# Kernel optimization log

Measured on AMD Instinct MI355X. Metric: run time of the kernel, lower is better.

The kernel has to match this reference:

```python
import jax, jax.numpy as jnp
import numpy as np

HEADS = 8
CPH = 32


def _rel_pos_indices(h, w):
    # same construction as the torch buffer, done statically in numpy
    coords = np.stack(np.meshgrid(np.arange(h), np.arange(w), indexing='ij')).reshape(2, -1)  # [2, N]
    rel = coords[:, :, None] - coords[:, None, :]  # [2, N, N]
    idx = (rel[0] + h - 1) * (2 * w - 1) + (rel[1] + w - 1)  # [N, N]
    return jnp.asarray(idx, dtype=jnp.int32)


def setup_inputs() -> dict:
    key = jax.random.key(0)
    ks = jax.random.split(key, 6)
    B, C, H, W = 2, 256, 48, 48
    emb = HEADS * CPH  # 256
    x = jax.random.normal(ks[0], (B, C, H, W), dtype=jnp.float32)
    # GDN params (kept positive so sqrt is well-defined)
    gdn_beta = jnp.ones((C,), dtype=jnp.float32)
    gdn_gamma = 0.1 * jnp.eye(C, dtype=jnp.float32) + 0.001 * jax.random.uniform(ks[1], (C, C), dtype=jnp.float32)
    w_qkv = 0.02 * jax.random.normal(ks[2], (3 * emb, C), dtype=jnp.float32)
    w_out = 0.02 * jax.random.normal(ks[3], (C, emb), dtype=jnp.float32)
    b_out = jnp.zeros((C,), dtype=jnp.float32)
    table_size = (2 * H - 1) * (2 * W - 1)
    rel_bias_table = 0.02 * jax.random.normal(ks[4], (table_size, HEADS), dtype=jnp.float32)
    return {"x": x, "gdn_beta": gdn_beta, "gdn_gamma": gdn_gamma,
            "w_qkv": w_qkv, "w_out": w_out, "b_out": b_out,
            "rel_bias_table": rel_bias_table}


def reference(x, gdn_beta, gdn_gamma, w_qkv, w_out, b_out, rel_bias_table):
    B, C, H, W = x.shape
    N = H * W
    emb = HEADS * CPH
    scale = CPH ** (-0.5)

    # GDN: y = x / sqrt(beta + gamma * x^2)  (1x1 conv over channels of x^2)
    norm = jnp.einsum('bchw,dc->bdhw', x * x, gdn_gamma) + gdn_beta[None, :, None, None]
    xn = x / jnp.sqrt(norm)

    # flatten spatial, channels last: [B, N, C]
    t = xn.reshape(B, C, N).transpose(0, 2, 1)

    # qkv projection (no bias)
    qkv = (t @ w_qkv.T).reshape(B, N, 3, HEADS, CPH).transpose(2, 0, 3, 1, 4)  # [3, B, h, N, d]
    q, k, v = qkv[0], qkv[1], qkv[2]

    attn = jnp.einsum('bhnd,bhmd->bhnm', q, k) * scale  # [B, h, N, N]

    # gathered relative position bias: [h, N, N]
    idx = _rel_pos_indices(H, W)  # [N, N], static ints
    bias = rel_bias_table[idx.reshape(-1)].reshape(N, N, HEADS).transpose(2, 0, 1)
    attn = jax.nn.softmax(attn + bias[None], axis=-1)

    # NOTE: faithful to the original quirk — reshape (B, h, N, d) directly
    # to (B, N, C) with NO head/seq transpose, exactly like the torch code.
    res = jnp.einsum('bhnm,bhmd->bhnd', attn, v).reshape(B, N, emb)

    out = res @ w_out.T + b_out  # [B, N, C]
    return out.transpose(0, 2, 1).reshape(B, C, H, W)
```

## Files before the change

### kernel.cpp

```cpp
#include <hip/hip_runtime.h>
#include <cstdint>
#include <cstddef>

typedef __attribute__((ext_vector_type(8))) short short8;
typedef __attribute__((ext_vector_type(4))) float floatx4;
typedef __attribute__((ext_vector_type(4))) unsigned short ushort4v;

#define NB 2
#define NPIX 2304
#define TBL 9025
#define TBLP 9032
#define L2E 1.4426950408889634f
#define QSCALE 0.17677669529663689f

__device__ __forceinline__ float b2f(unsigned short u) {
  union { unsigned int i; float f; } v; v.i = ((unsigned int)u) << 16; return v.f;
}
__device__ __forceinline__ unsigned short f2b(float f) {
  union { float f; unsigned int i; } v; v.f = f;
  return (unsigned short)((v.i + 0x7fffu + ((v.i >> 16) & 1u)) >> 16);
}
__device__ __forceinline__ unsigned int f2b2_fast(float lo, float hi) {
  union { float f; unsigned int i; } a, b; a.f = lo; b.f = hi;
  return ((a.i + 0x8000u) >> 16) | (((b.i + 0x8000u) >> 16) << 16);
}

__global__ __launch_bounds__(256) void prep_k(
    const float* __restrict__ gamma, const float* __restrict__ wqkv,
    const float* __restrict__ wout, const float* __restrict__ table,
    unsigned short* __restrict__ gb, unsigned short* __restrict__ qb,
    unsigned short* __restrict__ wb, float* __restrict__ tbf)
{
  int i = blockIdx.x * 256 + threadIdx.x;
  if (i < 65536)  gb[i] = f2b(gamma[i]);
  if (i < 196608) qb[i] = f2b(wqkv[i]);
  if (i < 65536)  wb[i] = f2b(wout[i]);
  if (i < TBL * 8) {
    int e = i >> 3, h = i & 7;
    tbf[(size_t)h * TBLP + e] = table[i] * L2E;
  }
}

template<int MODE>
__global__ __launch_bounds__(256) void gemm_k(
    const unsigned short* __restrict__ A,
    const void* __restrict__ Bv,
    const float* __restrict__ vec,
    unsigned short* __restrict__ o0,
    unsigned short* __restrict__ o1,
    unsigned short* __restrict__ o2,
    float* __restrict__ of)
{
  __shared__ unsigned short Al[64][40];
  __shared__ unsigned short Bl[64][40];
  const float* __restrict__ X = (const float*)Bv;
  const unsigned short* __restrict__ Bw = (const unsigned short*)Bv;

  const int n0 = blockIdx.x * 64;
  const int m0 = blockIdx.y * 64;
  const int b  = blockIdx.z;
  const int tid = threadIdx.x;
  const int wave = tid >> 6, lane = tid & 63;
  const int wm = wave >> 1, wn = wave & 1;
  const int lm = lane & 15, quad = lane >> 4;

  floatx4 acc[2][2] = {};

  for (int k0 = 0; k0 < 256; k0 += 32) {
    __syncthreads();
    {
      int ml = tid >> 2, ko = (tid & 3) * 8;
      *(short8*)&Al[ml][ko] = *(const short8*)&A[(size_t)(m0 + ml) * 256 + k0 + ko];
    }
    if (MODE == 0) {
      int kk = tid >> 3, n8 = (tid & 7) * 8;
      const float* xr = &X[((size_t)(b * 256 + k0 + kk)) * NPIX + n0 + n8];
      float4 x0 = *(const float4*)xr;
      float4 x1 = *(const float4*)(xr + 4);
      Bl[n8 + 0][kk] = f2b(x0.x * x0.x);
      Bl[n8 + 1][kk] = f2b(x0.y * x0.y);
      Bl[n8 + 2][kk] = f2b(x0.z * x0.z);
      Bl[n8 + 3][kk] = f2b(x0.w * x0.w);
      Bl[n8 + 4][kk] = f2b(x1.x * x1.x);
      Bl[n8 + 5][kk] = f2b(x1.y * x1.y);
      Bl[n8 + 6][kk] = f2b(x1.z * x1.z);
      Bl[n8 + 7][kk] = f2b(x1.w * x1.w);
    } else {
      int nl = tid >> 2, ko = (tid & 3) * 8;
      short8 bv = *(const short8*)&Bw[((size_t)b * NPIX + n0 + nl) * 256 + k0 + ko];
      *(short8*)&Bl[nl][ko] = bv;
    }
    __syncthreads();
    short8 af[2], bfr[2];
    #pragma unroll
    for (int tm = 0; tm < 2; ++tm)
      af[tm] = *(const short8*)&Al[wm*32 + tm*16 + lm][quad*8];
    #pragma unroll
    for (int tn = 0; tn < 2; ++tn)
      bfr[tn] = *(const short8*)&Bl[wn*32 + tn*16 + lm][quad*8];
    #pragma unroll
    for (int tm = 0; tm < 2; ++tm)
      #pragma unroll
      for (int tn = 0; tn < 2; ++tn)
        acc[tm][tn] = __builtin_amdgcn_mfma_f32_16x16x32_bf16(af[tm], bfr[tn], acc[tm][tn], 0, 0, 0);
  }

  #pragma unroll
  for (int tm = 0; tm < 2; ++tm) {
    const int rbase = m0 + wm*32 + tm*16 + quad*4;
    #pragma unroll
    for (int tn = 0; tn < 2; ++tn) {
      const int col = n0 + wn*32 + tn*16 + lm;
      floatx4 a4 = acc[tm][tn];
      if (MODE == 0) {
        ushort4v pk;
        #pragma unroll
        for (int r = 0; r < 4; ++r) {
          int d = rbase + r;
          float xv = X[((size_t)(b * 256 + d)) * NPIX + col];
          pk[r] = f2b(xv * rsqrtf(vec[d] + a4[r]));
        }
        *(ushort4v*)&o0[((size_t)(b * NPIX + col)) * 256 + rbase] = pk;
      } else if (MODE == 1) {
        const int part = rbase >> 8, h = (rbase >> 5) & 7, dd = rbase & 31;
        if (part == 2) {
          #pragma unroll
          for (int r = 0; r < 4; ++r)
            o2[(((size_t)(b * 8 + h)) * 32 + dd + r) * NPIX + col] = f2b(a4[r]);
        } else {
          unsigned short* dst = part == 0 ? o0 : o1;
          const float sc = (part == 0) ? (QSCALE * L2E) : 1.0f;
          ushort4v pk;
          #pragma unroll
          for (int r = 0; r < 4; ++r) pk[r] = f2b(a4[r] * sc);
          *(ushort4v*)&dst[(((size_t)(b * 8 + h)) * NPIX + col) * 32 + dd] = pk;
        }
      } else {
        #pragma unroll
        for (int r = 0; r < 4; ++r) {
          int c = rbase + r;
          of[((size_t)(b * 256 + c)) * NPIX + col] = a4[r] + vec[c];
        }
      }
    }
  }
}

__global__ __launch_bounds__(512, 4) void attn_k(
    const unsigned short* __restrict__ qg, const unsigned short* __restrict__ kg,
    const unsigned short* __restrict__ vt, const float* __restrict__ tabf_g,
    unsigned short* __restrict__ ob)
{
  __shared__ __align__(16) float tabf[TBLP];
  __shared__ __align__(16) float Om[8][16][36];
  __shared__ float lpart[2][4][16];

  const int tid = threadIdx.x;
  const int w = tid >> 6, lane = tid & 63;
  const int lm = lane & 15, quad = lane >> 4;
  const int gq = w & 3, half = w >> 2;
  const int bi = blockIdx.x;
  const int bh = (bi & 7) + 8 * ((bi >> 3) & 1);
  const int q0 = (bi >> 4) * 64;
  const size_t base = (size_t)bh * NPIX * 32;
  const int j00 = half * 1152;

  {
    const float* src = tabf_g + (size_t)(bh & 7) * TBLP;
    for (int e = tid * 4; e < TBLP; e += 2048)
      *(float4*)&tabf[e] = *(const float4*)&src[e];
  }
  __syncthreads();

  const int q = q0 + gq * 16 + lm;
  const short8 qfrag = *(const short8*)&qg[base + (size_t)q * 32 + quad * 8];

  const int hi = (q * 43691) >> 21;
  const int rb = (hi + 47) * 95 + (q - hi * 48) + 47;

  float lsum = 0.f;
  floatx4 o[2] = {};

  const int sA = lm + 16 * (2 * (quad & 1));
  const int ktsel = quad >> 1;

  for (int t = 0; t < 18; ++t) {
    const int j0 = j00 + t * 64;

    floatx4 s4[4];
    #pragma unroll
    for (int kt = 0; kt < 4; ++kt) {
      short8 kf = *(const short8*)&kg[base + (size_t)(j0 + kt * 16 + lm) * 32 + quad * 8];
      floatx4 z = {};
      s4[kt] = __builtin_amdgcn_mfma_f32_16x16x32_bf16(kf, qfrag, z, 0, 0, 0);
    }
    unsigned int pp[4][2];
    #pragma unroll
    for (int kt = 0; kt < 4; ++kt) {
      const int key0 = j0 + kt * 16 + quad * 4;
      const int hj = (key0 * 43691) >> 21;
      const int ib = rb - key0 - hj * 47;
      float p0 = __builtin_amdgcn_exp2f(s4[kt][0] + tabf[ib]);
      float p1 = __builtin_amdgcn_exp2f(s4[kt][1] + tabf[ib - 1]);
      float p2 = __builtin_amdgcn_exp2f(s4[kt][2] + tabf[ib - 2]);
      float p3 = __builtin_amdgcn_exp2f(s4[kt][3] + tabf[ib - 3]);
      lsum += (p0 + p1) + (p2 + p3);
      pp[kt][0] = f2b2_fast(p0, p1);
      pp[kt][1] = f2b2_fast(p2, p3);
    }
    #pragma unroll
    for (int c = 0; c < 2; ++c) {
      short8 pf;
      #pragma unroll
      for (int g = 0; g < 4; ++g) {
        const int sl = sA + 16 * (g >> 1);
        unsigned int u0 = (unsigned int)__shfl((int)pp[2 * c + 0][g & 1], sl, 64);
        unsigned int u1 = (unsigned int)__shfl((int)pp[2 * c + 1][g & 1], sl, 64);
        unsigned int u = ktsel ? u1 : u0;
        pf[2 * g]     = (short)(u & 0xffffu);
        pf[2 * g + 1] = (short)(u >> 16);
      }
      #pragma unroll
      for (int dt = 0; dt < 2; ++dt) {
        short8 vf = *(const short8*)&vt[base + (size_t)(dt * 16 + lm) * NPIX + j0 + c * 32 + quad * 8];
        o[dt] = __builtin_amdgcn_mfma_f32_16x16x32_bf16(vf, pf, o[dt], 0, 0, 0);
      }
    }
  }

  lsum += __shfl_xor(lsum, 16, 64);
  lsum += __shfl_xor(lsum, 32, 64);

  {
    const int row = half * 4 + gq;
    #pragma unroll
    for (int dt = 0; dt < 2; ++dt)
      *(floatx4*)&Om[row][lm][dt * 16 + quad * 4] = o[dt];
    if (quad == 0) lpart[half][gq][lm] = lsum;
  }
  __syncthreads();

  if (w < 4) {
    const int qq = lane >> 2, dg = lane & 3;
    const float inv = 1.f / (lpart[0][w][qq] + lpart[1][w][qq]);
    const float* r0 = &Om[w][qq][dg * 8];
    const float* r1 = &Om[4 + w][qq][dg * 8];
    short8 pk;
    #pragma unroll
    for (int r = 0; r < 8; ++r)
      pk[r] = (short)f2b((r0[r] + r1[r]) * inv);
    *(short8*)&ob[base + (size_t)(q0 + w * 16 + qq) * 32 + dg * 8] = pk;
  }
}

extern "C" void kernel_launch(void* const* d_in, const int* in_sizes, int n_in,
                              void* d_out, int out_size, void* d_ws, size_t ws_size,
                              hipStream_t stream) {
  const float* x     = (const float*)d_in[0];
  const float* beta  = (const float*)d_in[1];
  const float* gamma = (const float*)d_in[2];
  const float* wqkv  = (const float*)d_in[3];
  const float* wout  = (const float*)d_in[4];
  const float* bout  = (const float*)d_in[5];
  const float* table = (const float*)d_in[6];
  float* out = (float*)d_out;

  unsigned short* ws = (unsigned short*)d_ws;
  const size_t NE = (size_t)NB * NPIX * 256;
  unsigned short* xn_t  = ws;
  unsigned short* qbuf  = ws + NE;
  unsigned short* kbuf  = ws + 2 * NE;
  unsigned short* vtbuf = ws + 3 * NE;
  unsigned short* obuf  = ws + 4 * NE;
  unsigned short* gam_b = obuf;
  unsigned short* qkv_b = obuf + 65536;
  unsigned short* out_b = ws + 5 * NE;
  float* tab_f = (float*)(ws + 5 * NE + 65536);

  prep_k<<<768, 256, 0, stream>>>(gamma, wqkv, wout, table, gam_b, qkv_b, out_b, tab_f);
  gemm_k<0><<<dim3(36, 4, 2), 256, 0, stream>>>(gam_b, x, beta, xn_t, nullptr, nullptr, nullptr);
  gemm_k<1><<<dim3(36, 12, 2), 256, 0, stream>>>(qkv_b, xn_t, nullptr, qbuf, kbuf, vtbuf, nullptr);
  attn_k<<<576, 512, 0, stream>>>(qbuf, kbuf, vtbuf, tab_f, obuf);
  gemm_k<2><<<dim3(36, 4, 2), 256, 0, stream>>>(out_b, obuf, bout, nullptr, nullptr, nullptr, out);
}
```

Baseline: 172.0 us.

## Prefetch K/V/bias tiles in registers, pack bias pairs as bf16, use 16x16x16 MFMA for PV

```diff
diff --git a/kernel.cpp b/kernel.cpp
--- a/kernel.cpp
+++ b/kernel.cpp
@@ -3,8 +3,15 @@
 #include <cstddef>
 
 typedef __attribute__((ext_vector_type(8))) short short8;
+typedef __attribute__((ext_vector_type(4))) short short4v;
 typedef __attribute__((ext_vector_type(4))) float floatx4;
 typedef __attribute__((ext_vector_type(4))) unsigned short ushort4v;
+
+#if defined(__has_builtin)
+#  if __has_builtin(__builtin_amdgcn_mfma_f32_16x16x16bf16_1k)
+#    define HAVE_MFMA16 1
+#  endif
+#endif
 
 #define NB 2
 #define NPIX 2304
@@ -24,12 +31,18 @@
   union { float f; unsigned int i; } a, b; a.f = lo; b.f = hi;
   return ((a.i + 0x8000u) >> 16) | (((b.i + 0x8000u) >> 16) << 16);
 }
+__device__ __forceinline__ float hi2f(unsigned int u) {
+  union { unsigned int i; float f; } v; v.i = u & 0xffff0000u; return v.f;
+}
+__device__ __forceinline__ float lo2f(unsigned int u) {
+  union { unsigned int i; float f; } v; v.i = u << 16; return v.f;
+}
 
 __global__ __launch_bounds__(256) void prep_k(
     const float* __restrict__ gamma, const float* __restrict__ wqkv,
     const float* __restrict__ wout, const float* __restrict__ table,
     unsigned short* __restrict__ gb, unsigned short* __restrict__ qb,
-    unsigned short* __restrict__ wb, float* __restrict__ tbf)
+    unsigned short* __restrict__ wb, unsigned int* __restrict__ tabp)
 {
   int i = blockIdx.x * 256 + threadIdx.x;
   if (i < 65536)  gb[i] = f2b(gamma[i]);
@@ -37,7 +50,10 @@
   if (i < 65536)  wb[i] = f2b(wout[i]);
   if (i < TBL * 8) {
     int e = i >> 3, h = i & 7;
-    tbf[(size_t)h * TBLP + e] = table[i] * L2E;
+    int e1 = (e + 1 < TBL) ? e + 1 : e;
+    unsigned int lo = f2b(table[(size_t)e * 8 + h] * L2E);
+    unsigned int hi = f2b(table[(size_t)e1 * 8 + h] * L2E);
+    tabp[(size_t)h * TBLP + e] = lo | (hi << 16);
   }
 }
 
@@ -148,10 +164,9 @@
 
 __global__ __launch_bounds__(512, 4) void attn_k(
     const unsigned short* __restrict__ qg, const unsigned short* __restrict__ kg,
-    const unsigned short* __restrict__ vt, const float* __restrict__ tabf_g,
+    const unsigned short* __restrict__ vt, const unsigned int* __restrict__ tabp_g,
     unsigned short* __restrict__ ob)
 {
-  __shared__ __align__(16) float tabf[TBLP];
   __shared__ __align__(16) float Om[8][16][36];
   __shared__ float lpart[2][4][16];
 
@@ -164,13 +179,7 @@
   const int q0 = (bi >> 4) * 64;
   const size_t base = (size_t)bh * NPIX * 32;
   const int j00 = half * 1152;
-
-  {
-    const float* src = tabf_g + (size_t)(bh & 7) * TBLP;
-    for (int e = tid * 4; e < TBLP; e += 2048)
-      *(float4*)&tabf[e] = *(const float4*)&src[e];
-  }
-  __syncthreads();
+  const unsigned int* __restrict__ tp = tabp_g + (size_t)(bh & 7) * TBLP;
 
   const int q = q0 + gq * 16 + lm;
   const short8 qfrag = *(const short8*)&qg[base + (size_t)q * 32 + quad * 8];
@@ -181,33 +190,105 @@
   float lsum = 0.f;
   floatx4 o[2] = {};
 
+  short8 kf[4];
+#ifdef HAVE_MFMA16
+  short4v vf[8];
+#else
+  short8 vf[4];
   const int sA = lm + 16 * (2 * (quad & 1));
   const int ktsel = quad >> 1;
+#endif
+  unsigned int bd[8];
+
+  #pragma unroll
+  for (int kt = 0; kt < 4; ++kt)
+    kf[kt] = *(const short8*)&kg[base + (size_t)(j00 + kt * 16 + lm) * 32 + quad * 8];
+#ifdef HAVE_MFMA16
+  #pragma unroll
+  for (int kt = 0; kt < 4; ++kt)
+    #pragma unroll
+    for (int dt = 0; dt < 2; ++dt)
+      vf[kt * 2 + dt] = *(const short4v*)&vt[base + (size_t)(dt * 16 + lm) * NPIX + j00 + kt * 16 + quad * 4];
+#else
+  #pragma unroll
+  for (int c = 0; c < 2; ++c)
+    #pragma unroll
+    for (int dt = 0; dt < 2; ++dt)
+      vf[c * 2 + dt] = *(const short8*)&vt[base + (size_t)(dt * 16 + lm) * NPIX + j00 + c * 32 + quad * 8];
+#endif
+  #pragma unroll
+  for (int kt = 0; kt < 4; ++kt) {
+    const int key0 = j00 + kt * 16 + quad * 4;
+    const int hj = (key0 * 43691) >> 21;
+    const int ib = rb - key0 - hj * 47;
+    bd[kt * 2 + 0] = tp[ib - 1];
+    bd[kt * 2 + 1] = tp[ib - 3];
+  }
 
   for (int t = 0; t < 18; ++t) {
     const int j0 = j00 + t * 64;
-
-    floatx4 s4[4];
+    const int j0n = j00 + (t < 17 ? t + 1 : t) * 64;
+
+    short8 kn[4];
+#ifdef HAVE_MFMA16
+    short4v vn[8];
+#else
+    short8 vn[4];
+#endif
+    unsigned int bn[8];
+    #pragma unroll
+    for (int kt = 0; kt < 4; ++kt)
+      kn[kt] = *(const short8*)&kg[base + (size_t)(j0n + kt * 16 + lm) * 32 + quad * 8];
+#ifdef HAVE_MFMA16
+    #pragma unroll
+    for (int kt = 0; kt < 4; ++kt)
+      #pragma unroll
+      for (int dt = 0; dt < 2; ++dt)
+        vn[kt * 2 + dt] = *(const short4v*)&vt[base + (size_t)(dt * 16 + lm) * NPIX + j0n + kt * 16 + quad * 4];
+#else
+    #pragma unroll
+    for (int c = 0; c < 2; ++c)
+      #pragma unroll
+      for (int dt = 0; dt < 2; ++dt)
+        vn[c * 2 + dt] = *(const short8*)&vt[base + (size_t)(dt * 16 + lm) * NPIX + j0n + c * 32 + quad * 8];
+#endif
     #pragma unroll
     for (int kt = 0; kt < 4; ++kt) {
-      short8 kf = *(const short8*)&kg[base + (size_t)(j0 + kt * 16 + lm) * 32 + quad * 8];
-      floatx4 z = {};
-      s4[kt] = __builtin_amdgcn_mfma_f32_16x16x32_bf16(kf, qfrag, z, 0, 0, 0);
-    }
-    unsigned int pp[4][2];
-    #pragma unroll
-    for (int kt = 0; kt < 4; ++kt) {
-      const int key0 = j0 + kt * 16 + quad * 4;
+      const int key0 = j0n + kt * 16 + quad * 4;
       const int hj = (key0 * 43691) >> 21;
       const int ib = rb - key0 - hj * 47;
-      float p0 = __builtin_amdgcn_exp2f(s4[kt][0] + tabf[ib]);
-      float p1 = __builtin_amdgcn_exp2f(s4[kt][1] + tabf[ib - 1]);
-      float p2 = __builtin_amdgcn_exp2f(s4[kt][2] + tabf[ib - 2]);
-      float p3 = __builtin_amdgcn_exp2f(s4[kt][3] + tabf[ib - 3]);
+      bn[kt * 2 + 0] = tp[ib - 1];
+      bn[kt * 2 + 1] = tp[ib - 3];
+    }
+
+    floatx4 s4[4];
+    #pragma unroll
+    for (int kt = 0; kt < 4; ++kt) {
+      floatx4 z = {};
+      s4[kt] = __builtin_amdgcn_mfma_f32_16x16x32_bf16(kf[kt], qfrag, z, 0, 0, 0);
+    }
+    unsigned int pp[4][2];
+    #pragma unroll
+    for (int kt = 0; kt < 4; ++kt) {
+      const unsigned int d0 = bd[kt * 2 + 0], d1 = bd[kt * 2 + 1];
+      float p0 = __builtin_amdgcn_exp2f(s4[kt][0] + hi2f(d0));
+      float p1 = __builtin_amdgcn_exp2f(s4[kt][1] + lo2f(d0));
+      float p2 = __builtin_amdgcn_exp2f(s4[kt][2] + hi2f(d1));
+      float p3 = __builtin_amdgcn_exp2f(s4[kt][3] + lo2f(d1));
       lsum += (p0 + p1) + (p2 + p3);
       pp[kt][0] = f2b2_fast(p0, p1);
       pp[kt][1] = f2b2_fast(p2, p3);
     }
+#ifdef HAVE_MFMA16
+    #pragma unroll
+    for (int kt = 0; kt < 4; ++kt) {
+      unsigned int pr[2] = { pp[kt][0], pp[kt][1] };
+      short4v pf = *(short4v*)pr;
+      #pragma unroll
+      for (int dt = 0; dt < 2; ++dt)
+        o[dt] = __builtin_amdgcn_mfma_f32_16x16x16bf16_1k(vf[kt * 2 + dt], pf, o[dt], 0, 0, 0);
+    }
+#else
     #pragma unroll
     for (int c = 0; c < 2; ++c) {
       short8 pf;
@@ -221,11 +302,21 @@
         pf[2 * g + 1] = (short)(u >> 16);
       }
       #pragma unroll
-      for (int dt = 0; dt < 2; ++dt) {
-        short8 vf = *(const short8*)&vt[base + (size_t)(dt * 16 + lm) * NPIX + j0 + c * 32 + quad * 8];
-        o[dt] = __builtin_amdgcn_mfma_f32_16x16x32_bf16(vf, pf, o[dt], 0, 0, 0);
-      }
-    }
+      for (int dt = 0; dt < 2; ++dt)
+        o[dt] = __builtin_amdgcn_mfma_f32_16x16x32_bf16(vf[c * 2 + dt], pf, o[dt], 0, 0, 0);
+    }
+#endif
+    #pragma unroll
+    for (int i2 = 0; i2 < 4; ++i2) kf[i2] = kn[i2];
+#ifdef HAVE_MFMA16
+    #pragma unroll
+    for (int i2 = 0; i2 < 8; ++i2) vf[i2] = vn[i2];
+#else
+    #pragma unroll
+    for (int i2 = 0; i2 < 4; ++i2) vf[i2] = vn[i2];
+#endif
+    #pragma unroll
+    for (int i2 = 0; i2 < 8; ++i2) bd[i2] = bn[i2];
   }
 
   lsum += __shfl_xor(lsum, 16, 64);
@@ -275,11 +366,11 @@
   unsigned short* gam_b = obuf;
   unsigned short* qkv_b = obuf + 65536;
   unsigned short* out_b = ws + 5 * NE;
-  float* tab_f = (float*)(ws + 5 * NE + 65536);
-
-  prep_k<<<768, 256, 0, stream>>>(gamma, wqkv, wout, table, gam_b, qkv_b, out_b, tab_f);
+  unsigned int* tab_p = (unsigned int*)(ws + 5 * NE + 65536);
+
+  prep_k<<<768, 256, 0, stream>>>(gamma, wqkv, wout, table, gam_b, qkv_b, out_b, tab_p);
   gemm_k<0><<<dim3(36, 4, 2), 256, 0, stream>>>(gam_b, x, beta, xn_t, nullptr, nullptr, nullptr);
   gemm_k<1><<<dim3(36, 12, 2), 256, 0, stream>>>(qkv_b, xn_t, nullptr, qbuf, kbuf, vtbuf, nullptr);
-  attn_k<<<576, 512, 0, stream>>>(qbuf, kbuf, vtbuf, tab_f, obuf);
+  attn_k<<<576, 512, 0, stream>>>(qbuf, kbuf, vtbuf, tab_p, obuf);
   gemm_k<2><<<dim3(36, 4, 2), 256, 0, stream>>>(out_b, obuf, bout, nullptr, nullptr, nullptr, out);
 }
```

After: 221.8 us. 1.29x slower.
